# Kernel optimization log

Hardware: AMD Instinct MI355X
Metric: run time of the kernel (lower is better)

The kernel has to match this reference:

```python
import jax, jax.numpy as jnp
import numpy as np

N, M_DIM, CTRL = 16384, 512, 1024
EPS = 1e-16

def setup_inputs() -> dict:
    key = jax.random.key(0)
    k1, k2, k3, k4, k5 = jax.random.split(key, 5)
    embeddings = jax.random.normal(k1, (1, CTRL), dtype=jnp.float32)
    w_prev = jax.random.uniform(k2, (1, N), dtype=jnp.float32)
    w_prev = w_prev / jnp.sum(w_prev, axis=1, keepdims=True)  # valid soft address
    memory = jax.random.normal(k3, (N, M_DIM), dtype=jnp.float32) * 0.05
    out_f = 3 * M_DIM + 6  # write_lengths = [M,1,1,3,1,M,M]
    W = jax.random.normal(k4, (out_f, CTRL), dtype=jnp.float32) * (1.0 / np.sqrt(CTRL))
    b = jax.random.normal(k5, (out_f,), dtype=jnp.float32) * 0.01
    return {"embeddings": embeddings, "w_prev": w_prev, "memory": memory, "W": W, "b": b}

def reference(embeddings, w_prev, memory, W, b):
    Md = memory.shape[1]
    o = (embeddings @ W.T + b).reshape(1, -1)  # [1, 3M+6]
    # column split per write_lengths [M,1,1,3,1,M,M]
    k = o[:, :Md]
    beta = jax.nn.softplus(o[:, Md:Md + 1])
    g = jax.nn.sigmoid(o[:, Md + 1:Md + 2])
    s = jax.nn.softmax(o[:, Md + 2:Md + 5], axis=1)       # 3 circular shifts
    gamma = 1.0 + jax.nn.softplus(o[:, Md + 5:Md + 6])
    e = o[:, Md + 6:2 * Md + 6]                            # erase vector [1,M]
    a = o[:, 2 * Md + 6:]                                  # add vector   [1,M]
    # content addressing: cosine similarity of k against each memory row
    mem_norm = jnp.linalg.norm(memory, axis=1)             # [N]
    k_norm = jnp.linalg.norm(k, axis=1)                    # [1]
    sim = (k @ memory.T) / (k_norm[:, None] * mem_norm[None, :] + EPS)  # [1,N]
    wc = jax.nn.softmax(beta * sim, axis=1)
    # interpolation with previous weights
    wg = g * wc + (1.0 - g) * w_prev
    # circular convolution with 3-tap shift kernel (shifts -1,0,+1)
    ws = (s[:, 0:1] * jnp.roll(wg, 1, axis=1)
          + s[:, 1:2] * wg
          + s[:, 2:3] * jnp.roll(wg, -1, axis=1))
    # sharpening
    wp = jnp.power(ws + EPS, gamma)
    w = wp / jnp.sum(wp, axis=1, keepdims=True)            # [1,N]
    # erase/add outer-product memory write
    erase = w.T @ e                                        # [N,M]
    add = w.T @ a                                          # [N,M]
    new_memory = memory * (1.0 - erase) + add
    return w, new_memory
```

## Files before the change

### kernel.cpp

```cpp
#include <hip/hip_runtime.h>
#include <math.h>

#define N 16384
#define MD 512
#define CTRLDIM 1024
#define OUTF 1542


__device__ __forceinline__ float softplus_f(float x) {
    return (x > 20.f) ? x : log1pf(expf(x));
}

__device__ __forceinline__ float wave_bfly_sum(float v) {
    #pragma unroll
    for (int off = 1; off < 64; off <<= 1) v += __shfl_xor(v, off, 64);
    return v;
}

__global__ void k_proj(const float* __restrict__ emb, const float* __restrict__ W,
                       const float* __restrict__ b, float* __restrict__ O,
                       float* __restrict__ E, float* __restrict__ A) {
    int row = blockIdx.x;
    int t = threadIdx.x;
    const float4* w4 = (const float4*)(W + (size_t)row * CTRLDIM);
    const float4* e4 = (const float4*)emb;
    float4 wv = w4[t];
    float4 ev = e4[t];
    float p = wv.x * ev.x + wv.y * ev.y + wv.z * ev.z + wv.w * ev.w;
    p = wave_bfly_sum(p);
    __shared__ float s[4];
    int lane = t & 63, wid = t >> 6;
    if (lane == 0) s[wid] = p;
    __syncthreads();
    if (t == 0) {
        float val = s[0] + s[1] + s[2] + s[3] + b[row];
        O[row] = val;
        if (row >= MD + 6 && row < 2 * MD + 6)      E[row - (MD + 6)] = val;
        else if (row >= 2 * MD + 6)                 A[row - (2 * MD + 6)] = val;
    }
}

__global__ void __launch_bounds__(256) k_sim(const float* __restrict__ mem,
                                             const float* __restrict__ O,
                                             float* __restrict__ EZ,
                                             float* __restrict__ PART1) {
    int t = threadIdx.x, lane = t & 63, wid = t >> 6;
    const float4* k4 = (const float4*)O;
    float4 k0 = k4[lane], k1 = k4[lane + 64];
    float ksq = k0.x * k0.x + k0.y * k0.y + k0.z * k0.z + k0.w * k0.w
              + k1.x * k1.x + k1.y * k1.y + k1.z * k1.z + k1.w * k1.w;
    ksq = wave_bfly_sum(ksq);
    float knorm = sqrtf(ksq);
    float beta = softplus_f(O[MD]);
    int row0 = (blockIdx.x * 4 + wid) * 8;
    float4 m0[8], m1[8];
    #pragma unroll
    for (int r = 0; r < 8; r++) {
        const float4* m4 = (const float4*)(mem + (size_t)(row0 + r) * MD);
        m0[r] = m4[lane];
        m1[r] = m4[lane + 64];
    }
    float wsum = 0.f;
    #pragma unroll
    for (int r = 0; r < 8; r++) {
        float dot = m0[r].x * k0.x + m0[r].y * k0.y + m0[r].z * k0.z + m0[r].w * k0.w
                  + m1[r].x * k1.x + m1[r].y * k1.y + m1[r].z * k1.z + m1[r].w * k1.w;
        float nsq = m0[r].x * m0[r].x + m0[r].y * m0[r].y + m0[r].z * m0[r].z + m0[r].w * m0[r].w
                  + m1[r].x * m1[r].x + m1[r].y * m1[r].y + m1[r].z * m1[r].z + m1[r].w * m1[r].w;
        dot = wave_bfly_sum(dot);
        nsq = wave_bfly_sum(nsq);
        float z = beta * dot / (knorm * sqrtf(nsq) + 1e-16f);
        float ez = expf(z - beta);
        if (lane == r) EZ[row0 + r] = ez;
        wsum += ez;
    }
    __shared__ float sblk[4];
    if (lane == 0) sblk[wid] = wsum;
    __syncthreads();
    if (t == 0) PART1[blockIdx.x] = sblk[0] + sblk[1] + sblk[2] + sblk[3];
}

__global__ void __launch_bounds__(512) k_supd(const float* __restrict__ mem,
                                              const float* __restrict__ EZ,
                                              const float* __restrict__ wprev,
                                              const float* __restrict__ O,
                                              const float* __restrict__ PART1,
                                              const float* __restrict__ E,
                                              const float* __restrict__ A,
                                              float* __restrict__ wout,
                                              float* __restrict__ outMem) {
    int t = threadIdx.x, lane = t & 63, wid = t >> 6;
    int b = blockIdx.x;
    __shared__ float lds_wp[64];
    __shared__ float sblk[8];

    float v = PART1[lane] + PART1[lane + 64] + PART1[lane + 128] + PART1[lane + 192]
            + PART1[lane + 256] + PART1[lane + 320] + PART1[lane + 384] + PART1[lane + 448];
    float inv1 = 1.f / wave_bfly_sum(v);

    float g = 1.f / (1.f + expf(-O[MD + 1]));
    float s0r = O[MD + 2], s1r = O[MD + 3], s2r = O[MD + 4];
    float m = fmaxf(s0r, fmaxf(s1r, s2r));
    float e0 = expf(s0r - m), e1 = expf(s1r - m), e2 = expf(s2r - m);
    float inv_se = 1.f / (e0 + e1 + e2);
    float s0 = e0 * inv_se, s1 = e1 * inv_se, s2 = e2 * inv_se;
    float gamma = 1.f + softplus_f(O[MD + 5]);
    float gm1 = 1.f - g;

    int jmine = b >> 3;
    int tlo = (b & 7) * 64;
    float sum2 = 0.f;
    #pragma unroll 4
    for (int j = 0; j < N / 512; j++) {
        int i = j * 512 + t;
        int im = (i == 0) ? (N - 1) : (i - 1);
        int ip = (i == N - 1) ? 0 : (i + 1);
        float wgm = g * EZ[im] * inv1 + gm1 * wprev[im];
        float wgc = g * EZ[i]  * inv1 + gm1 * wprev[i];
        float wgp = g * EZ[ip] * inv1 + gm1 * wprev[ip];
        float wsv = s0 * wgm + s1 * wgc + s2 * wgp;
        float wp = exp2f(gamma * log2f(wsv + 1e-16f));
        sum2 += wp;
        if (j == jmine && t >= tlo && t < tlo + 64) lds_wp[t - tlo] = wp;
    }
    float bs = wave_bfly_sum(sum2);
    if (lane == 0) sblk[wid] = bs;
    __syncthreads();
    float inv2 = 1.f / (sblk[0] + sblk[1] + sblk[2] + sblk[3]
                      + sblk[4] + sblk[5] + sblk[6] + sblk[7]);

    if (t < 64) wout[b * 64 + t] = lds_wp[t] * inv2;

    const float4* m4 = (const float4*)mem;
    const float4* e4 = (const float4*)E;
    const float4* a4 = (const float4*)A;
    float4* o4 = (float4*)outMem;
    #pragma unroll 4
    for (int it = 0; it < 16; it++) {
        int local = it * 512 + t;
        int idx = b * 8192 + local;
        float wi = lds_wp[local >> 7] * inv2;
        int c = local & 127;
        float4 mv = m4[idx];
        float4 e = e4[c];
        float4 a = a4[c];
        float4 o;
        o.x = mv.x * (1.f - wi * e.x) + wi * a.x;
        o.y = mv.y * (1.f - wi * e.y) + wi * a.y;
        o.z = mv.z * (1.f - wi * e.z) + wi * a.z;
        o.w = mv.w * (1.f - wi * e.w) + wi * a.w;
        o4[idx] = o;
    }
}

extern "C" void kernel_launch(void* const* d_in, const int* in_sizes, int n_in,
                              void* d_out, int out_size, void* d_ws, size_t ws_size,
                              hipStream_t stream) {
    const float* emb   = (const float*)d_in[0];
    const float* wprev = (const float*)d_in[1];
    const float* mem   = (const float*)d_in[2];
    const float* W     = (const float*)d_in[3];
    const float* b     = (const float*)d_in[4];
    float* out = (float*)d_out;
    float* wsf = (float*)d_ws;
    float* O     = wsf;
    float* E     = wsf + 1552;
    float* A     = wsf + 2064;
    float* PART1 = wsf + 2576;
    float* EZ    = wsf + 3664;

    k_proj<<<OUTF, 256, 0, stream>>>(emb, W, b, O, E, A);
    k_sim<<<N / 32, 256, 0, stream>>>(mem, O, EZ, PART1);
    k_supd<<<256, 512, 0, stream>>>(mem, EZ, wprev, O, PART1, E, A, out, out + N);
}
```

Baseline: 119.9 us.

## Double k_supd grid and stage interpolated weights in LDS for shift convolution

Launches twice as many update blocks, each handling 32 memory rows instead of 64, to spread the memory-write phase across more workgroups. The three-tap circular shift now stages interpolated weights for each 512-element tile in a double-buffered LDS array with halo cells, avoiding three global loads and recomputations per element. The trade-off is that every block still recomputes the full normalization sum, so doubling the block count doubles that redundant work, and the tile loop now needs a barrier per iteration.

```diff
diff --git a/kernel.cpp b/kernel.cpp
--- a/kernel.cpp
+++ b/kernel.cpp
@@ -91,11 +91,13 @@
                                               float* __restrict__ outMem) {
     int t = threadIdx.x, lane = t & 63, wid = t >> 6;
     int b = blockIdx.x;
-    __shared__ float lds_wp[64];
+    __shared__ float lds_wg[2][514];
+    __shared__ float lds_wp[32];
     __shared__ float sblk[8];
 
-    float v = PART1[lane] + PART1[lane + 64] + PART1[lane + 128] + PART1[lane + 192]
-            + PART1[lane + 256] + PART1[lane + 320] + PART1[lane + 384] + PART1[lane + 448];
+    float v = 0.f;
+    #pragma unroll
+    for (int j = 0; j < 8; j++) v += PART1[lane + j * 64];
     float inv1 = 1.f / wave_bfly_sum(v);
 
     float g = 1.f / (1.f + expf(-O[MD + 1]));
@@ -105,23 +107,30 @@
     float inv_se = 1.f / (e0 + e1 + e2);
     float s0 = e0 * inv_se, s1 = e1 * inv_se, s2 = e2 * inv_se;
     float gamma = 1.f + softplus_f(O[MD + 5]);
+    float gi1 = g * inv1;
     float gm1 = 1.f - g;
 
-    int jmine = b >> 3;
-    int tlo = (b & 7) * 64;
+    int jmine = b >> 4;
+    int tlo = (b & 15) * 32;
+
     float sum2 = 0.f;
-    #pragma unroll 4
     for (int j = 0; j < N / 512; j++) {
-        int i = j * 512 + t;
-        int im = (i == 0) ? (N - 1) : (i - 1);
-        int ip = (i == N - 1) ? 0 : (i + 1);
-        float wgm = g * EZ[im] * inv1 + gm1 * wprev[im];
-        float wgc = g * EZ[i]  * inv1 + gm1 * wprev[i];
-        float wgp = g * EZ[ip] * inv1 + gm1 * wprev[ip];
-        float wsv = s0 * wgm + s1 * wgc + s2 * wgp;
+        float* buf = lds_wg[j & 1];
+        int base = j * 512;
+        int i = base + t;
+        buf[t + 1] = gi1 * EZ[i] + gm1 * wprev[i];
+        if (t == 0) {
+            int il = (base == 0) ? (N - 1) : (base - 1);
+            buf[0] = gi1 * EZ[il] + gm1 * wprev[il];
+        } else if (t == 1) {
+            int ir = (base + 512 == N) ? 0 : (base + 512);
+            buf[513] = gi1 * EZ[ir] + gm1 * wprev[ir];
+        }
+        __syncthreads();
+        float wsv = s0 * buf[t] + s1 * buf[t + 1] + s2 * buf[t + 2];
         float wp = exp2f(gamma * log2f(wsv + 1e-16f));
         sum2 += wp;
-        if (j == jmine && t >= tlo && t < tlo + 64) lds_wp[t - tlo] = wp;
+        if (j == jmine && t >= tlo && t < tlo + 32) lds_wp[t - tlo] = wp;
     }
     float bs = wave_bfly_sum(sum2);
     if (lane == 0) sblk[wid] = bs;
@@ -129,16 +138,16 @@
     float inv2 = 1.f / (sblk[0] + sblk[1] + sblk[2] + sblk[3]
                       + sblk[4] + sblk[5] + sblk[6] + sblk[7]);
 
-    if (t < 64) wout[b * 64 + t] = lds_wp[t] * inv2;
+    if (t < 32) wout[b * 32 + t] = lds_wp[t] * inv2;
 
     const float4* m4 = (const float4*)mem;
     const float4* e4 = (const float4*)E;
     const float4* a4 = (const float4*)A;
     float4* o4 = (float4*)outMem;
-    #pragma unroll 4
-    for (int it = 0; it < 16; it++) {
+    #pragma unroll
+    for (int it = 0; it < 8; it++) {
         int local = it * 512 + t;
-        int idx = b * 8192 + local;
+        int idx = b * 4096 + local;
         float wi = lds_wp[local >> 7] * inv2;
         int c = local & 127;
         float4 mv = m4[idx];
@@ -171,5 +180,5 @@
 
     k_proj<<<OUTF, 256, 0, stream>>>(emb, W, b, O, E, A);
     k_sim<<<N / 32, 256, 0, stream>>>(mem, O, EZ, PART1);
-    k_supd<<<256, 512, 0, stream>>>(mem, EZ, wprev, O, PART1, E, A, out, out + N);
+    k_supd<<<512, 512, 0, stream>>>(mem, EZ, wprev, O, PART1, E, A, out, out + N);
 }
```

Measured after the change: 136.0 us. 1.13x slower.
